# Performance work log

Hardware: AMD Instinct MI355X
Metric: run time of the kernel (lower is better)

Reference implementation:

```python
import jax, jax.numpy as jnp
import numpy as np

J = 1.0          # coupling constant
PT_PERIOD = 4    # parallel-tempering exchange every PT_PERIOD sweeps


def setup_inputs() -> dict:
    key = jax.random.key(0)
    k1, k2 = jax.random.split(key)
    B, C, L = 32, 16, 256
    # temperatures across the Ising critical region, sorted ascending
    T = jnp.sort(1.5 + 2.0 * jax.random.uniform(k1, (B,), dtype=jnp.float32))
    # spins stored as {0,1} ints; converted to +/-1 inside reference
    spins = jax.random.randint(k2, (B, C, L, L), 0, 2).astype(jnp.int32)
    return {"T": T, "spins": spins, "n_sweeps": 16}


def _neighbor_sum(s):
    # periodic 4-neighbor sum, shape preserved [B,C,L,L]
    return (jnp.roll(s, 1, -1) + jnp.roll(s, -1, -1)
            + jnp.roll(s, 1, -2) + jnp.roll(s, -1, -2))


def _energy(s):
    # total Ising energy per chain: -J * sum_<ij> s_i s_j  -> [B, C]
    return -J * jnp.sum(s * (jnp.roll(s, -1, -1) + jnp.roll(s, -1, -2)), axis=(-1, -2))


def reference(T, spins, n_sweeps):
    B, C, L, _ = spins.shape
    s = spins.astype(jnp.float32) * 2.0 - 1.0          # +/-1 spins
    ii = jnp.arange(L)
    parity = (ii[:, None] + ii[None, :]) % 2            # [L,L] checkerboard
    Tb = T[:, None, None, None]                         # [B,1,1,1]
    beta = 1.0 / T                                      # [B]
    base_key = jax.random.key(42)

    def half_sweep(s, key, color):
        dE = 2.0 * J * s * _neighbor_sum(s)             # local energy change on flip
        u = jax.random.uniform(key, s.shape, dtype=jnp.float32)
        acc = u < jnp.exp(-dE / Tb)                     # Metropolis accept
        mask = (parity == color)                        # update one sub-lattice only
        return jnp.where(mask & acc, -s, s)

    def pt_swap(s, key, pair_parity):
        # attempt swaps between adjacent temperatures (b, b+1) with given pair parity
        E = _energy(s)                                  # [B, C]
        d = (beta[:-1] - beta[1:])[:, None] * (E[:-1] - E[1:])   # [B-1, C]
        u = jax.random.uniform(key, (B - 1, C), dtype=jnp.float32)
        pair_mask = (jnp.arange(B - 1) % 2) == pair_parity
        acc = (u < jnp.exp(d)) & pair_mask[:, None]     # [B-1, C] non-overlapping
        swap_next = jnp.concatenate([acc, jnp.zeros((1, C), bool)], 0)  # swap b<->b+1
        swap_prev = jnp.concatenate([jnp.zeros((1, C), bool), acc], 0)
        s_next = jnp.roll(s, -1, axis=0)
        s_prev = jnp.roll(s, 1, axis=0)
        swn = swap_next[:, :, None, None]
        swp = swap_prev[:, :, None, None]
        return jnp.where(swn, s_next, jnp.where(swp, s_prev, s))

    def sweep(s, t):
        kb = jax.random.fold_in(base_key, t)
        k1, k2, k3 = jax.random.split(kb, 3)
        s = half_sweep(s, k1, 0)   # black sub-lattice
        s = half_sweep(s, k2, 1)   # white sub-lattice
        do_pt = (t % PT_PERIOD) == (PT_PERIOD - 1)
        s = jax.lax.cond(do_pt,
                         lambda s_: pt_swap(s_, k3, (t // PT_PERIOD) % 2),
                         lambda s_: s_, s)
        return s, None

    s, _ = jax.lax.scan(sweep, s, jnp.arange(n_sweeps))
    return s, _energy(s)
```

## Files before the change

### kernel.cpp

```cpp
#include <hip/hip_runtime.h>
#include <stdint.h>


#define BB 32
#define CC 16
#define PLANE 65536
#define NSITE (BB * CC * PLANE)
#define NPAIR ((BB - 1) * CC)

__host__ __device__ __forceinline__ void tf2x32(uint32_t k0, uint32_t k1,
                                                uint32_t c0, uint32_t c1,
                                                uint32_t& o0, uint32_t& o1) {
  uint32_t ks2 = k0 ^ k1 ^ 0x1BD11BDAu;
  uint32_t x0 = c0 + k0;
  uint32_t x1 = c1 + k1;
#define TF_ROT(r) { x0 += x1; x1 = (x1 << (r)) | (x1 >> (32 - (r))); x1 ^= x0; }
  TF_ROT(13) TF_ROT(15) TF_ROT(26) TF_ROT(6)
  x0 += k1;  x1 += ks2 + 1u;
  TF_ROT(17) TF_ROT(29) TF_ROT(16) TF_ROT(24)
  x0 += ks2; x1 += k0 + 2u;
  TF_ROT(13) TF_ROT(15) TF_ROT(26) TF_ROT(6)
  x0 += k0;  x1 += k1 + 3u;
  TF_ROT(17) TF_ROT(29) TF_ROT(16) TF_ROT(24)
  x0 += k1;  x1 += ks2 + 4u;
  TF_ROT(13) TF_ROT(15) TF_ROT(26) TF_ROT(6)
  x0 += ks2; x1 += k0 + 5u;
#undef TF_ROT
  o0 = x0; o1 = x1;
}

__device__ __forceinline__ uint32_t rotl(uint32_t x, int r) {
  return __builtin_amdgcn_alignbit(x, x, 32 - r);
}

__device__ __forceinline__ uint32_t tf_bits(uint32_t k0, uint32_t k1,
                                            uint32_t ks2, uint32_t x1i) {
  uint32_t x0 = k0, x1 = x1i;
#define R4(a,b,c,d) \
  x0 += x1; x1 = rotl(x1, (a)); x1 ^= x0; \
  x0 += x1; x1 = rotl(x1, (b)); x1 ^= x0; \
  x0 += x1; x1 = rotl(x1, (c)); x1 ^= x0; \
  x0 += x1; x1 = rotl(x1, (d)); x1 ^= x0;
  R4(13,15,26,6)  x0 += k1;  x1 += ks2 + 1u;
  R4(17,29,16,24) x0 += ks2; x1 += k0 + 2u;
  R4(13,15,26,6)  x0 += k0;  x1 += k1 + 3u;
  R4(17,29,16,24) x0 += k1;  x1 += ks2 + 4u;
  R4(13,15,26,6)  x0 += ks2; x1 += k0 + 5u;
#undef R4
  return x0 ^ x1;
}

__device__ __forceinline__ float u01(uint32_t bits) {
  return __uint_as_float((bits >> 9) | 0x3f800000u) - 1.0f;
}

__device__ __forceinline__ bool pt_accept(int pair, const float* Eplane,
                                          const float* T,
                                          uint32_t k0, uint32_t k1) {
  int b = pair >> 4;
  float d = (1.0f / T[b] - 1.0f / T[b + 1])
          * (Eplane[pair] - Eplane[pair + 16]);
  uint32_t h0, h1;
  tf2x32(k0, k1, 0u, (uint32_t)pair, h0, h1);
  float u = u01(h0 ^ h1);
  float th = (float)exp((double)d);
  return u < th;
}

__global__ __launch_bounds__(256) void init8_prep_k(
    const int* __restrict__ spins, uint8_t* __restrict__ s,
    const float* __restrict__ T,
    uint32_t* __restrict__ M4, uint32_t* __restrict__ M8) {
  int i = blockIdx.x * 256 + threadIdx.x;
  int4 v = ((const int4*)spins)[i];
  uint32_t o = ((uint32_t)(uint8_t)(int8_t)(2 * v.x - 1))
             | ((uint32_t)(uint8_t)(int8_t)(2 * v.y - 1) << 8)
             | ((uint32_t)(uint8_t)(int8_t)(2 * v.z - 1) << 16)
             | ((uint32_t)(uint8_t)(int8_t)(2 * v.w - 1) << 24);
  ((uint32_t*)s)[i] = o;
  if (blockIdx.x == 0 && threadIdx.x < BB) {
    int b = threadIdx.x;
    float t = T[b];
    float th4 = (float)exp((double)((-4.0f) / t));
    float th8 = (float)exp((double)((-8.0f) / t));
    M4[b] = (uint32_t)ceil((double)th4 * 8388608.0);
    M8[b] = (uint32_t)ceil((double)th8 * 8388608.0);
  }
}

__device__ __forceinline__ void do_color(uint32_t* __restrict__ tile,
    int w, int lane, int lm, int lp, uint32_t vk, int color,
    uint32_t k0, uint32_t k1, uint32_t ks2, uint32_t M4b, uint32_t M8b) {
#pragma unroll 4
  for (int it = 0; it < 16; ++it) {
    int j  = w + it * 16;
    int rb = j << 6;
    int ju = ((j + 255) & 255) << 6;
    int jd = ((j + 1) & 255) << 6;
    int p  = (j + color) & 1;
    uint32_t soff = (uint32_t)((j << 8) + p);

    uint32_t cur = tile[rb + lane];
    uint32_t up  = tile[ju + lane];
    uint32_t dn  = tile[jd + lane];
    uint32_t pw  = tile[rb + lm];
    uint32_t nw  = tile[rb + lp];
    uint32_t lft = __builtin_amdgcn_alignbit(cur, pw, 24);
    uint32_t rgt = __builtin_amdgcn_alignbit(nw, cur, 8);
    uint32_t kd2 = (up & 0x02020202u) + (dn & 0x02020202u)
                 + (lft & 0x02020202u) + (rgt & 0x02020202u);

    uint32_t flip = 0;
    {
      uint32_t kdi = (kd2 >> (8 * p)) & 0xFFu;
      uint32_t si  = (cur >> (8 * p + 1)) & 1u;
      uint32_t m2  = si ? (8u - kdi) : kdi;
      bool a = true;
      if (m2 < 4u) {
        uint32_t n = tf_bits(k0, k1, ks2, vk + soff) >> 9;
        a = n < (m2 == 2u ? M4b : M8b);
      }
      if (a) flip |= 0xFEu << (8 * p);
    }
    {
      uint32_t kdi = (kd2 >> (8 * p + 16)) & 0xFFu;
      uint32_t si  = (cur >> (8 * p + 17)) & 1u;
      uint32_t m2  = si ? (8u - kdi) : kdi;
      bool a = true;
      if (m2 < 4u) {
        uint32_t n = tf_bits(k0, k1, ks2, vk + soff + 2u) >> 9;
        a = n < (m2 == 2u ? M4b : M8b);
      }
      if (a) flip |= 0xFE0000u << (8 * p);
    }
    tile[rb + lane] = cur ^ flip;
  }
}

__global__ __launch_bounds__(1024) void sweep4_k(
    uint8_t* __restrict__ sg,
    const uint32_t* __restrict__ M4, const uint32_t* __restrict__ M8,
    uint4 kS0, uint4 kS1, uint4 kS2, uint4 kS3,
    int tbase, const int* __restrict__ nsw, float* __restrict__ Eplane) {
  __shared__ uint32_t tile[16384];
  int tid = threadIdx.x;
  int bc  = blockIdx.x;
  int b   = bc >> 4;
  uint32_t bcbase = (uint32_t)bc << 16;
  uint32_t* gp = (uint32_t*)(sg + ((size_t)bc << 16));
  uint32_t M4b = M4[b], M8b = M8[b];
  int nswv = *nsw;

  for (int i = tid; i < 4096; i += 1024)
    ((uint4*)tile)[i] = ((const uint4*)gp)[i];
  __syncthreads();

  int w    = __builtin_amdgcn_readfirstlane(tid >> 6);
  int lane = tid & 63;
  int lm   = (lane + 63) & 63, lp = (lane + 1) & 63;

  uint4 keys[4] = {kS0, kS1, kS2, kS3};
#pragma unroll
  for (int ss = 0; ss < 4; ++ss) {
    if (tbase + ss < nswv) {
      uint32_t kA0 = keys[ss].x, kA1 = keys[ss].y;
      uint32_t kB0 = keys[ss].z, kB1 = keys[ss].w;
      uint32_t ksA = kA0 ^ kA1 ^ 0x1BD11BDAu;
      uint32_t ksB = kB0 ^ kB1 ^ 0x1BD11BDAu;
      uint32_t vkA = kA1 + bcbase + (uint32_t)(lane << 2);
      uint32_t vkB = kB1 + bcbase + (uint32_t)(lane << 2);
      do_color(tile, w, lane, lm, lp, vkA, 0, kA0, kA1, ksA, M4b, M8b);
      __syncthreads();
      do_color(tile, w, lane, lm, lp, vkB, 1, kB0, kB1, ksB, M4b, M8b);
      __syncthreads();
    }
  }

  int acc = 0;
  for (int it = 0; it < 16; ++it) {
    int j = w + it * 16;
    uint32_t cur = tile[(j << 6) + lane];
    uint32_t nxt = tile[(j << 6) + lp];
    uint32_t dwn = tile[((((j + 1) & 255)) << 6) + lane];
    uint32_t rsh = (cur >> 8) | (nxt << 24);
    int d = __builtin_popcount((cur ^ rsh) & 0x02020202u)
          + __builtin_popcount((cur ^ dwn) & 0x02020202u);
    acc += 8 - 2 * d;
  }

  for (int i = tid; i < 4096; i += 1024)
    ((uint4*)gp)[i] = ((uint4*)tile)[i];
  __syncthreads();

  for (int off = 32; off > 0; off >>= 1) acc += __shfl_down(acc, off, 64);
  if (lane == 0) tile[w] = (uint32_t)acc;
  __syncthreads();
  if (tid == 0) {
    int tot = 0;
    for (int i = 0; i < 16; ++i) tot += (int)tile[i];
    Eplane[bc] = -(float)tot;
  }
}

__global__ __launch_bounds__(256) void pt_swapD_k(uint8_t* __restrict__ s,
    const float* __restrict__ Eplane, const float* __restrict__ T,
    uint32_t k0, uint32_t k1, int pair_parity, int t,
    const int* __restrict__ nsw) {
  int pc = blockIdx.x;
  int b  = pc >> 4;
  if ((b & 1) != pair_parity) return;
  if (t >= *nsw) return;
  if (!pt_accept(pc, Eplane, T, k0, k1)) return;
  uint4* p0 = (uint4*)(s + ((size_t)pc << 16));
  uint4* p1 = p0 + (CC * PLANE / 16);
  for (int j = threadIdx.x; j < PLANE / 16; j += 256) {
    uint4 a0 = p0[j], a1 = p1[j];
    p0[j] = a1; p1[j] = a0;
  }
}

__device__ __forceinline__ int perm_src(int pc, const float* Eplane,
                                        const float* T, uint32_t k0,
                                        uint32_t k1, int pair_parity,
                                        int t, int nswv) {
  int b = pc >> 4;
  if (t < nswv) {
    if (b < 31 && (b & 1) == pair_parity &&
        pt_accept(pc, Eplane, T, k0, k1)) return pc + 16;
    if (b > 0 && ((b - 1) & 1) == pair_parity &&
        pt_accept(pc - 16, Eplane, T, k0, k1)) return pc - 16;
  }
  return pc;
}

__global__ __launch_bounds__(256) void permute_out_k(
    const uint8_t* __restrict__ s, uint8_t* __restrict__ dst,
    const float* __restrict__ Eplane, const float* __restrict__ T,
    uint32_t k0, uint32_t k1, int pair_parity, int t,
    const int* __restrict__ nsw, float* __restrict__ Eout) {
  int pc = blockIdx.x;
  int src = perm_src(pc, Eplane, T, k0, k1, pair_parity, t, *nsw);
  const uint4* p0 = (const uint4*)(s + ((size_t)src << 16));
  uint4*       p1 = (uint4*)(dst + ((size_t)pc << 16));
  for (int j = threadIdx.x; j < PLANE / 16; j += 256)
    p1[j] = p0[j];
  if (threadIdx.x == 0) Eout[pc] = Eplane[src];
}

__global__ __launch_bounds__(256) void expand_full_k(
    const uint8_t* __restrict__ st, float* __restrict__ out) {
  int i = blockIdx.x * 256 + threadIdx.x;
  uint32_t v = ((const uint32_t*)st)[i];
  float4 o;
  o.x = (float)(int8_t)(v);
  o.y = (float)(int8_t)(v >> 8);
  o.z = (float)(int8_t)(v >> 16);
  o.w = (float)(int8_t)(v >> 24);
  ((float4*)out)[i] = o;
}

__global__ void final_eoutD_k(const float* __restrict__ Eplane,
                              const float* __restrict__ T,
                              uint32_t k0, uint32_t k1, int pair_parity,
                              int t, const int* __restrict__ nsw,
                              float* __restrict__ Eout) {
  int pc = threadIdx.x;
  int src = perm_src(pc, Eplane, T, k0, k1, pair_parity, t, *nsw);
  Eout[pc] = Eplane[src];
}

__global__ __launch_bounds__(256) void expand_k(const int8_t* __restrict__ st,
                                                float* __restrict__ out,
                                                int lo, int cnt4) {
  int i = blockIdx.x * 256 + threadIdx.x;
  if (i >= cnt4) return;
  uint32_t v = *(const uint32_t*)(st + lo + 4 * i);
  float4 o;
  o.x = (float)(int8_t)(v);
  o.y = (float)(int8_t)(v >> 8);
  o.z = (float)(int8_t)(v >> 16);
  o.w = (float)(int8_t)(v >> 24);
  ((float4*)out)[(lo >> 2) + i] = o;
}

__global__ __launch_bounds__(256) void expand_head_k(const int8_t* __restrict__ st,
                                                     float* __restrict__ out) {
  uint32_t r[8];
  int t = threadIdx.x;
  for (int u = 0; u < 8; ++u) r[u] = *(const uint32_t*)(st + t * 32 + 4 * u);
  __syncthreads();
  for (int u = 0; u < 8; ++u) {
    uint32_t v = r[u];
    float4 o;
    o.x = (float)(int8_t)(v);
    o.y = (float)(int8_t)(v >> 8);
    o.z = (float)(int8_t)(v >> 16);
    o.w = (float)(int8_t)(v >> 24);
    ((float4*)out)[t * 8 + u] = o;
  }
}

extern "C" void kernel_launch(void* const* d_in, const int* in_sizes, int n_in,
                              void* d_out, int out_size, void* d_ws, size_t ws_size,
                              hipStream_t stream) {
  (void)in_sizes; (void)n_in; (void)out_size;
  const float* T    = (const float*)d_in[0];
  const int*  spins = (const int*)d_in[1];
  const int*  nsw   = (const int*)d_in[2];

  uint8_t* buf0 = (uint8_t*)d_out;
  float*   outf = (float*)d_out;
  float*   Eout = outf + NSITE;

  float*    Eplane = (float*)d_ws;
  uint32_t* M4     = (uint32_t*)(Eplane + 512);
  uint32_t* M8     = M4 + BB;
  uint8_t*  wstate = (uint8_t*)d_ws + 4096;
  bool big_ws = (ws_size >= (size_t)NSITE + 4096);

  init8_prep_k<<<NSITE / 1024, 256, 0, stream>>>(spins, buf0, T, M4, M8);

  uint32_t k3fa = 0, k3fb = 0;
  for (int g = 0; g < 4; ++g) {
    uint4 kS[4];
    uint32_t k3a = 0, k3b = 0;
    for (int i = 0; i < 4; ++i) {
      int t = 4 * g + i;
      uint32_t kb0, kb1;
      tf2x32(0u, 42u, 0u, (uint32_t)t, kb0, kb1);
      tf2x32(kb0, kb1, 0u, 0u, kS[i].x, kS[i].y);
      tf2x32(kb0, kb1, 0u, 1u, kS[i].z, kS[i].w);
      if (i == 3) tf2x32(kb0, kb1, 0u, 2u, k3a, k3b);
    }
    sweep4_k<<<BB * CC, 1024, 0, stream>>>(buf0, M4, M8,
                                           kS[0], kS[1], kS[2], kS[3],
                                           4 * g, nsw, Eplane);
    if (g < 3) {
      pt_swapD_k<<<NPAIR, 256, 0, stream>>>(buf0, Eplane, T, k3a, k3b,
                                            g & 1, 4 * g + 3, nsw);
    } else {
      k3fa = k3a; k3fb = k3b;
    }
  }

  if (big_ws) {
    permute_out_k<<<BB * CC, 256, 0, stream>>>(buf0, wstate, Eplane, T,
                                               k3fa, k3fb, 1, 15, nsw, Eout);
    expand_full_k<<<NSITE / 1024, 256, 0, stream>>>(wstate, outf);
  } else {
    pt_swapD_k<<<NPAIR, 256, 0, stream>>>(buf0, Eplane, T, k3fa, k3fb,
                                          1, 15, nsw);
    final_eoutD_k<<<1, 512, 0, stream>>>(Eplane, T, k3fa, k3fb, 1, 15,
                                         nsw, Eout);
    for (int lo = NSITE / 4; lo >= 8192; lo >>= 2) {
      int cnt4 = (lo * 3) / 4;
      expand_k<<<(cnt4 + 255) / 256, 256, 0, stream>>>((int8_t*)buf0, outf,
                                                       lo, cnt4);
    }
    expand_head_k<<<1, 256, 0, stream>>>((int8_t*)buf0, outf);
  }
}
```

Baseline: 1.454 ms.

## Fuse spin init into first sweep and permutation into final expand

The separate int-to-int8 init kernel is removed: the first sweep kernel now reads the int32 spins directly into shared memory, and each block computes its own Metropolis thresholds from T. On the large-workspace path, the final permute-copy and expand kernels are merged into one kernel that reads the permuted source plane and writes floats directly. This removes two kernel launches and a full int8 round trip through global memory, at the cost of redundant threshold computation per block.

```diff
diff --git a/kernel.cpp b/kernel.cpp
--- a/kernel.cpp
+++ b/kernel.cpp
@@ -54,6 +54,14 @@
   return __uint_as_float((bits >> 9) | 0x3f800000u) - 1.0f;
 }
 
+__device__ __forceinline__ void mk_thresholds(float tb, uint32_t& M4b,
+                                              uint32_t& M8b) {
+  float th4 = (float)exp((double)((-4.0f) / tb));
+  float th8 = (float)exp((double)((-8.0f) / tb));
+  M4b = (uint32_t)ceil((double)th4 * 8388608.0);
+  M8b = (uint32_t)ceil((double)th8 * 8388608.0);
+}
+
 __device__ __forceinline__ bool pt_accept(int pair, const float* Eplane,
                                           const float* T,
                                           uint32_t k0, uint32_t k1) {
@@ -67,27 +75,6 @@
   return u < th;
 }
 
-__global__ __launch_bounds__(256) void init8_prep_k(
-    const int* __restrict__ spins, uint8_t* __restrict__ s,
-    const float* __restrict__ T,
-    uint32_t* __restrict__ M4, uint32_t* __restrict__ M8) {
-  int i = blockIdx.x * 256 + threadIdx.x;
-  int4 v = ((const int4*)spins)[i];
-  uint32_t o = ((uint32_t)(uint8_t)(int8_t)(2 * v.x - 1))
-             | ((uint32_t)(uint8_t)(int8_t)(2 * v.y - 1) << 8)
-             | ((uint32_t)(uint8_t)(int8_t)(2 * v.z - 1) << 16)
-             | ((uint32_t)(uint8_t)(int8_t)(2 * v.w - 1) << 24);
-  ((uint32_t*)s)[i] = o;
-  if (blockIdx.x == 0 && threadIdx.x < BB) {
-    int b = threadIdx.x;
-    float t = T[b];
-    float th4 = (float)exp((double)((-4.0f) / t));
-    float th8 = (float)exp((double)((-8.0f) / t));
-    M4[b] = (uint32_t)ceil((double)th4 * 8388608.0);
-    M8[b] = (uint32_t)ceil((double)th8 * 8388608.0);
-  }
-}
-
 __device__ __forceinline__ void do_color(uint32_t* __restrict__ tile,
     int w, int lane, int lm, int lp, uint32_t vk, int color,
     uint32_t k0, uint32_t k1, uint32_t ks2, uint32_t M4b, uint32_t M8b) {
@@ -138,8 +125,8 @@
 }
 
 __global__ __launch_bounds__(1024) void sweep4_k(
-    uint8_t* __restrict__ sg,
-    const uint32_t* __restrict__ M4, const uint32_t* __restrict__ M8,
+    uint8_t* __restrict__ sg, const int* __restrict__ spins, int doInit,
+    const float* __restrict__ T,
     uint4 kS0, uint4 kS1, uint4 kS2, uint4 kS3,
     int tbase, const int* __restrict__ nsw, float* __restrict__ Eplane) {
   __shared__ uint32_t tile[16384];
@@ -148,11 +135,23 @@
   int b   = bc >> 4;
   uint32_t bcbase = (uint32_t)bc << 16;
   uint32_t* gp = (uint32_t*)(sg + ((size_t)bc << 16));
-  uint32_t M4b = M4[b], M8b = M8[b];
+  uint32_t M4b, M8b;
+  mk_thresholds(T[b], M4b, M8b);
   int nswv = *nsw;
 
-  for (int i = tid; i < 4096; i += 1024)
-    ((uint4*)tile)[i] = ((const uint4*)gp)[i];
+  if (doInit) {
+    const int4* ip = (const int4*)(spins + ((size_t)bc << 16));
+    for (int i = tid; i < 16384; i += 1024) {
+      int4 v = ip[i];
+      tile[i] = ((uint32_t)(uint8_t)(int8_t)(2 * v.x - 1))
+              | ((uint32_t)(uint8_t)(int8_t)(2 * v.y - 1) << 8)
+              | ((uint32_t)(uint8_t)(int8_t)(2 * v.z - 1) << 16)
+              | ((uint32_t)(uint8_t)(int8_t)(2 * v.w - 1) << 24);
+    }
+  } else {
+    for (int i = tid; i < 4096; i += 1024)
+      ((uint4*)tile)[i] = ((const uint4*)gp)[i];
+  }
   __syncthreads();
 
   int w    = __builtin_amdgcn_readfirstlane(tid >> 6);
@@ -233,30 +232,27 @@
   return pc;
 }
 
-__global__ __launch_bounds__(256) void permute_out_k(
-    const uint8_t* __restrict__ s, uint8_t* __restrict__ dst,
+__global__ __launch_bounds__(256) void expand_perm_k(
+    const uint8_t* __restrict__ s, float* __restrict__ out,
     const float* __restrict__ Eplane, const float* __restrict__ T,
     uint32_t k0, uint32_t k1, int pair_parity, int t,
     const int* __restrict__ nsw, float* __restrict__ Eout) {
-  int pc = blockIdx.x;
+  int pc  = blockIdx.x >> 3;
+  int sub = blockIdx.x & 7;
   int src = perm_src(pc, Eplane, T, k0, k1, pair_parity, t, *nsw);
-  const uint4* p0 = (const uint4*)(s + ((size_t)src << 16));
-  uint4*       p1 = (uint4*)(dst + ((size_t)pc << 16));
-  for (int j = threadIdx.x; j < PLANE / 16; j += 256)
-    p1[j] = p0[j];
-  if (threadIdx.x == 0) Eout[pc] = Eplane[src];
-}
-
-__global__ __launch_bounds__(256) void expand_full_k(
-    const uint8_t* __restrict__ st, float* __restrict__ out) {
-  int i = blockIdx.x * 256 + threadIdx.x;
-  uint32_t v = ((const uint32_t*)st)[i];
-  float4 o;
-  o.x = (float)(int8_t)(v);
-  o.y = (float)(int8_t)(v >> 8);
-  o.z = (float)(int8_t)(v >> 16);
-  o.w = (float)(int8_t)(v >> 24);
-  ((float4*)out)[i] = o;
+  const uint32_t* p0 = (const uint32_t*)(s + ((size_t)src << 16));
+  float4* p1 = (float4*)(out + ((size_t)pc << 14));
+  int base = sub * 2048;
+  for (int j = threadIdx.x; j < 2048; j += 256) {
+    uint32_t v = p0[base + j];
+    float4 o;
+    o.x = (float)(int8_t)(v);
+    o.y = (float)(int8_t)(v >> 8);
+    o.z = (float)(int8_t)(v >> 16);
+    o.w = (float)(int8_t)(v >> 24);
+    p1[base + j] = o;
+  }
+  if (threadIdx.x == 0 && sub == 0) Eout[pc] = Eplane[src];
 }
 
 __global__ void final_eoutD_k(const float* __restrict__ Eplane,
@@ -308,17 +304,13 @@
   const int*  spins = (const int*)d_in[1];
   const int*  nsw   = (const int*)d_in[2];
 
-  uint8_t* buf0 = (uint8_t*)d_out;
-  float*   outf = (float*)d_out;
-  float*   Eout = outf + NSITE;
-
-  float*    Eplane = (float*)d_ws;
-  uint32_t* M4     = (uint32_t*)(Eplane + 512);
-  uint32_t* M8     = M4 + BB;
-  uint8_t*  wstate = (uint8_t*)d_ws + 4096;
+  float* outf = (float*)d_out;
+  float* Eout = outf + NSITE;
+
+  float*   Eplane = (float*)d_ws;
+  uint8_t* wstate = (uint8_t*)d_ws + 4096;
   bool big_ws = (ws_size >= (size_t)NSITE + 4096);
-
-  init8_prep_k<<<NSITE / 1024, 256, 0, stream>>>(spins, buf0, T, M4, M8);
+  uint8_t* state = big_ws ? wstate : (uint8_t*)d_out;
 
   uint32_t k3fa = 0, k3fb = 0;
   for (int g = 0; g < 4; ++g) {
@@ -332,11 +324,11 @@
       tf2x32(kb0, kb1, 0u, 1u, kS[i].z, kS[i].w);
       if (i == 3) tf2x32(kb0, kb1, 0u, 2u, k3a, k3b);
     }
-    sweep4_k<<<BB * CC, 1024, 0, stream>>>(buf0, M4, M8,
-                                           kS[0], kS[1], kS[2], kS[3],
+    sweep4_k<<<BB * CC, 1024, 0, stream>>>(state, spins, (g == 0) ? 1 : 0,
+                                           T, kS[0], kS[1], kS[2], kS[3],
                                            4 * g, nsw, Eplane);
     if (g < 3) {
-      pt_swapD_k<<<NPAIR, 256, 0, stream>>>(buf0, Eplane, T, k3a, k3b,
+      pt_swapD_k<<<NPAIR, 256, 0, stream>>>(state, Eplane, T, k3a, k3b,
                                             g & 1, 4 * g + 3, nsw);
     } else {
       k3fa = k3a; k3fb = k3b;
@@ -344,19 +336,19 @@
   }
 
   if (big_ws) {
-    permute_out_k<<<BB * CC, 256, 0, stream>>>(buf0, wstate, Eplane, T,
-                                               k3fa, k3fb, 1, 15, nsw, Eout);
-    expand_full_k<<<NSITE / 1024, 256, 0, stream>>>(wstate, outf);
+    expand_perm_k<<<BB * CC * 8, 256, 0, stream>>>(state, outf, Eplane, T,
+                                                   k3fa, k3fb, 1, 15, nsw,
+                                                   Eout);
   } else {
-    pt_swapD_k<<<NPAIR, 256, 0, stream>>>(buf0, Eplane, T, k3fa, k3fb,
+    pt_swapD_k<<<NPAIR, 256, 0, stream>>>(state, Eplane, T, k3fa, k3fb,
                                           1, 15, nsw);
     final_eoutD_k<<<1, 512, 0, stream>>>(Eplane, T, k3fa, k3fb, 1, 15,
                                          nsw, Eout);
     for (int lo = NSITE / 4; lo >= 8192; lo >>= 2) {
       int cnt4 = (lo * 3) / 4;
-      expand_k<<<(cnt4 + 255) / 256, 256, 0, stream>>>((int8_t*)buf0, outf,
+      expand_k<<<(cnt4 + 255) / 256, 256, 0, stream>>>((int8_t*)state, outf,
                                                        lo, cnt4);
     }
-    expand_head_k<<<1, 256, 0, stream>>>((int8_t*)buf0, outf);
-  }
-}
+    expand_head_k<<<1, 256, 0, stream>>>((int8_t*)state, outf);
+  }
+}
```

New measurement: 1.416 ms. 2.6% less time.
